# Kernel optimization log

Hardware: AMD Instinct MI355X
Metric: run time of the kernel (lower is better)

## Reference

```python
import jax, jax.numpy as jnp
import numpy as np

N_NODES = 100000
N_EDGES = 3200000
D_IN = 256   # module's size_out (input feature dim)
D_OUT = 128  # module's size_in (output feature dim)


def setup_inputs() -> dict:
    key = jax.random.key(0)
    k1, k2, k3, k4, k5 = jax.random.split(key, 5)
    x = jax.random.normal(k1, (N_NODES, D_IN), dtype=jnp.float32)
    W = jax.random.normal(k2, (D_IN, D_OUT), dtype=jnp.float32) * 0.05
    edge_src = jax.random.randint(k3, (N_EDGES,), 0, N_NODES, dtype=jnp.int32)
    edge_dst = jax.random.randint(k4, (N_EDGES,), 0, N_NODES, dtype=jnp.int32)
    edge_weight = jax.random.uniform(k5, (N_EDGES,), dtype=jnp.float32)
    return {"x": x, "W": W, "edge_src": edge_src, "edge_dst": edge_dst,
            "edge_weight": edge_weight}


def reference(x, W, edge_src, edge_dst, edge_weight):
    # dense projection: torch.mm(x, weights) -> [N, D_OUT]
    h = x @ W
    # sparse adjacency matmul: torch.spmm(A, h) with A in COO form
    # out[d] = sum_{e: dst_e = d} w_e * h[src_e]
    msgs = edge_weight[:, None] * h[edge_src]          # [E, D_OUT]
    out = jax.ops.segment_sum(msgs, edge_dst, num_segments=N_NODES)
    return out
```

## Files before the change

### kernel.cpp

```cpp
#include <hip/hip_runtime.h>

#define D_IN 256
#define D_OUT 128

typedef __bf16  bf16x8 __attribute__((ext_vector_type(8)));
typedef float   f32x4  __attribute__((ext_vector_type(4)));

__global__ __launch_bounds__(256) void wtrans_kernel(const float* __restrict__ W,
                                                     __bf16* __restrict__ Wt) {
    int n = blockIdx.x * 256 + threadIdx.x;
    int k = n >> 7;
    int col = n & 127;
    Wt[(size_t)col * D_IN + k] = (__bf16)W[(size_t)k * D_OUT + col];
}

__global__ __launch_bounds__(256) void gemm_mfma_kernel(const float* __restrict__ x,
                                                        const __bf16* __restrict__ Wt,
                                                        __bf16* __restrict__ h16, int M) {
    const int lane = threadIdx.x & 63;
    const int wid  = threadIdx.x >> 6;
    const int r0   = blockIdx.x * 128 + wid * 32;
    const int lr   = lane & 15;
    const int koff = (lane >> 4) * 8;

    int rowA = r0 + lr;        if (rowA >= M) rowA = M - 1;
    int rowB = r0 + 16 + lr;   if (rowB >= M) rowB = M - 1;
    const float* pa0 = &x[(size_t)rowA * D_IN + koff];
    const float* pa1 = &x[(size_t)rowB * D_IN + koff];

    f32x4 acc0[8], acc1[8];
#pragma unroll
    for (int c = 0; c < 8; ++c) { acc0[c] = (f32x4)0.f; acc1[c] = (f32x4)0.f; }

#pragma unroll
    for (int t = 0; t < 8; ++t) {
        float4 fa0 = *(const float4*)(pa0 + t * 32);
        float4 fa1 = *(const float4*)(pa0 + t * 32 + 4);
        float4 fb0 = *(const float4*)(pa1 + t * 32);
        float4 fb1 = *(const float4*)(pa1 + t * 32 + 4);
        bf16x8 aA, aB;
        aA[0]=(__bf16)fa0.x; aA[1]=(__bf16)fa0.y; aA[2]=(__bf16)fa0.z; aA[3]=(__bf16)fa0.w;
        aA[4]=(__bf16)fa1.x; aA[5]=(__bf16)fa1.y; aA[6]=(__bf16)fa1.z; aA[7]=(__bf16)fa1.w;
        aB[0]=(__bf16)fb0.x; aB[1]=(__bf16)fb0.y; aB[2]=(__bf16)fb0.z; aB[3]=(__bf16)fb0.w;
        aB[4]=(__bf16)fb1.x; aB[5]=(__bf16)fb1.y; aB[6]=(__bf16)fb1.z; aB[7]=(__bf16)fb1.w;
#pragma unroll
        for (int c = 0; c < 8; ++c) {
            bf16x8 b = *(const bf16x8*)&Wt[(size_t)(c * 16 + lr) * D_IN + t * 32 + koff];
            acc0[c] = __builtin_amdgcn_mfma_f32_16x16x32_bf16(aA, b, acc0[c], 0, 0, 0);
            acc1[c] = __builtin_amdgcn_mfma_f32_16x16x32_bf16(aB, b, acc1[c], 0, 0, 0);
        }
    }

    const int q = lane >> 4;
#pragma unroll
    for (int c = 0; c < 8; ++c) {
        int col = c * 16 + lr;
#pragma unroll
        for (int i = 0; i < 4; ++i) {
            int ra = r0 + q * 4 + i;
            int rb = r0 + 16 + q * 4 + i;
            if (ra < M) h16[(size_t)ra * D_OUT + col] = (__bf16)acc0[c][i];
            if (rb < M) h16[(size_t)rb * D_OUT + col] = (__bf16)acc1[c][i];
        }
    }
}

__global__ void hist_kernel(const int* __restrict__ dst, int* __restrict__ count, int E) {
    int i = blockIdx.x * blockDim.x + threadIdx.x;
    int stride = gridDim.x * blockDim.x;
    for (; i < E; i += stride) atomicAdd(&count[dst[i]], 1);
}

__global__ void scan1_kernel(const int* __restrict__ count, int* __restrict__ offsets,
                             int* __restrict__ bsum, int N) {
    __shared__ int s[256];
    int tid = threadIdx.x;
    int i = blockIdx.x * 256 + tid;
    int v = (i < N) ? count[i] : 0;
    s[tid] = v;
    __syncthreads();
    for (int off = 1; off < 256; off <<= 1) {
        int t = (tid >= off) ? s[tid - off] : 0;
        __syncthreads();
        s[tid] += t;
        __syncthreads();
    }
    if (i < N) offsets[i] = s[tid] - v;
    if (tid == 255) bsum[blockIdx.x] = s[255];
}

__global__ void scan2_kernel(const int* __restrict__ bsum, int* __restrict__ bscan, int NB) {
    __shared__ int s[512];
    int tid = threadIdx.x;
    int v = (tid < NB) ? bsum[tid] : 0;
    s[tid] = v;
    __syncthreads();
    for (int off = 1; off < 512; off <<= 1) {
        int t = (tid >= off) ? s[tid - off] : 0;
        __syncthreads();
        s[tid] += t;
        __syncthreads();
    }
    if (tid < NB) bscan[tid] = s[tid] - v;
}

__global__ void scan3_kernel(int* __restrict__ offsets, const int* __restrict__ bscan,
                             int* __restrict__ cursor, int N) {
    int i = blockIdx.x * blockDim.x + threadIdx.x;
    if (i < N) {
        int o = offsets[i] + bscan[i >> 8];
        offsets[i] = o;
        cursor[i]  = o;
    }
}

__global__ void scatter_kernel(const int* __restrict__ src, const int* __restrict__ dst,
                               const float* __restrict__ w, int* __restrict__ cursor,
                               int2* __restrict__ ep, int E) {
    int i = blockIdx.x * blockDim.x + threadIdx.x;
    int stride = gridDim.x * blockDim.x;
    for (; i < E; i += stride) {
        int d = dst[i];
        int pos = atomicAdd(&cursor[d], 1);
        ep[pos] = make_int2(src[i], __float_as_int(w[i]));
    }
}

__global__ __launch_bounds__(256) void spmm_kernel(const int* __restrict__ offsets,
                                                   const int* __restrict__ count,
                                                   const int2* __restrict__ ep,
                                                   const unsigned int* __restrict__ h16,
                                                   float* __restrict__ out, int N) {
    int wid  = (blockIdx.x * 256 + threadIdx.x) >> 6;
    int lane = threadIdx.x & 63;
    if (wid >= N) return;
    int start = offsets[wid];
    int cnt   = count[wid];
    float ax = 0.f, ay = 0.f;
    for (int j = 0; j < cnt; j += 8) {
        int2 e[8]; float wt[8];
#pragma unroll
        for (int k = 0; k < 8; ++k) {
            int jj = j + k;
            int idx = start + (jj < cnt ? jj : cnt - 1);
            e[k] = ep[idx];
            wt[k] = (jj < cnt) ? __int_as_float(e[k].y) : 0.f;
        }
        unsigned int u[8];
#pragma unroll
        for (int k = 0; k < 8; ++k)
            u[k] = h16[(size_t)e[k].x * 64 + lane];
#pragma unroll
        for (int k = 0; k < 8; ++k) {
            float flo = __uint_as_float(u[k] << 16);
            float fhi = __uint_as_float(u[k] & 0xffff0000u);
            ax += wt[k] * flo;
            ay += wt[k] * fhi;
        }
    }
    out[(size_t)wid * D_OUT + lane * 2 + 0] = ax;
    out[(size_t)wid * D_OUT + lane * 2 + 1] = ay;
}

__global__ __launch_bounds__(256) void edge_atomic_kernel(const int* __restrict__ src,
                                                          const int* __restrict__ dst,
                                                          const float* __restrict__ w,
                                                          const unsigned int* __restrict__ h16,
                                                          float* __restrict__ out, int E) {
    int wid  = (blockIdx.x * 256 + threadIdx.x) >> 6;
    int lane = threadIdx.x & 63;
    if (wid >= E) return;
    int s = src[wid], d = dst[wid];
    float ww = w[wid];
    unsigned int u = h16[(size_t)s * 64 + lane];
    atomicAdd(&out[(size_t)d * D_OUT + lane * 2 + 0], ww * __uint_as_float(u << 16));
    atomicAdd(&out[(size_t)d * D_OUT + lane * 2 + 1], ww * __uint_as_float(u & 0xffff0000u));
}

extern "C" void kernel_launch(void* const* d_in, const int* in_sizes, int n_in,
                              void* d_out, int out_size, void* d_ws, size_t ws_size,
                              hipStream_t stream) {
    const float* x    = (const float*)d_in[0];
    const float* W    = (const float*)d_in[1];
    const int*   esrc = (const int*)d_in[2];
    const int*   edst = (const int*)d_in[3];
    const float* ew   = (const float*)d_in[4];
    float* out = (float*)d_out;

    const int M = in_sizes[0] / D_IN;
    const int E = in_sizes[2];

    char* ws = (char*)d_ws;
    size_t off = 0;
    __bf16* h16    = (__bf16*)(ws + off); off += (size_t)M * D_OUT * 2;
    int2*   ep     = (int2*)  (ws + off); off += (size_t)E * 8;
    __bf16* Wt     = (__bf16*)(ws + off); off += (size_t)D_IN * D_OUT * 2;
    int*    offsets= (int*)   (ws + off); off += (size_t)M * 4;
    int*    count  = (int*)   (ws + off); off += (size_t)M * 4;
    int*    cursor = (int*)   (ws + off); off += (size_t)M * 4;
    int*    bsum   = (int*)   (ws + off); off += 2048;
    int*    bscan  = (int*)   (ws + off); off += 2048;
    const bool use_csr = (off <= ws_size);

    wtrans_kernel<<<(D_IN * D_OUT + 255) / 256, 256, 0, stream>>>(W, Wt);
    gemm_mfma_kernel<<<(M + 127) / 128, 256, 0, stream>>>(x, Wt, h16, M);

    if (use_csr) {
        int NB = (M + 255) / 256;
        hipMemsetAsync(count, 0, (size_t)M * 4, stream);
        hist_kernel  <<<2048, 256, 0, stream>>>(edst, count, E);
        scan1_kernel <<<NB, 256, 0, stream>>>(count, offsets, bsum, M);
        scan2_kernel <<<1, 512, 0, stream>>>(bsum, bscan, NB);
        scan3_kernel <<<NB, 256, 0, stream>>>(offsets, bscan, cursor, M);
        scatter_kernel<<<2048, 256, 0, stream>>>(esrc, edst, ew, cursor, ep, E);
        spmm_kernel  <<<(M + 3) / 4, 256, 0, stream>>>(offsets, count, ep,
                                                       (const unsigned int*)h16, out, M);
    } else {
        hipMemsetAsync(d_out, 0, (size_t)out_size * 4, stream);
        long long nthreads = (long long)E * 64;
        edge_atomic_kernel<<<(nthreads + 255) / 256, 256, 0, stream>>>(
            esrc, edst, ew, (const unsigned int*)h16, out, E);
    }
}
```

Before: 728.4 us.

## Record per-edge rank in histogram, make scatter atomic-free and XCD-partitioned by destination

The histogram pass now stores each edge's atomic return value as its rank within its destination segment, so the scatter pass computes positions as offsets[d]+rank[i] without a second round of atomics and the cursor array is dropped. Scatter blocks are split into 8 groups keyed on blockIdx&7, each owning a contiguous destination range, so that writes into ep from one group land in a localized region, presumably matching the XCD round-robin dispatch. Every group rereads the whole dst array, and an extra E-sized rank array is written and read. The SpMM inner loop is also unrolled from 8 to 16 edges per batch for more gathers in flight, at the cost of more wasted clamped loads on short rows and higher register pressure.

```diff
diff --git a/kernel.cpp b/kernel.cpp
--- a/kernel.cpp
+++ b/kernel.cpp
@@ -65,10 +65,11 @@
     }
 }
 
-__global__ void hist_kernel(const int* __restrict__ dst, int* __restrict__ count, int E) {
+__global__ void hist_kernel(const int* __restrict__ dst, int* __restrict__ count,
+                            int* __restrict__ rank, int E) {
     int i = blockIdx.x * blockDim.x + threadIdx.x;
     int stride = gridDim.x * blockDim.x;
-    for (; i < E; i += stride) atomicAdd(&count[dst[i]], 1);
+    for (; i < E; i += stride) rank[i] = atomicAdd(&count[dst[i]], 1);
 }
 
 __global__ void scan1_kernel(const int* __restrict__ count, int* __restrict__ offsets,
@@ -104,25 +105,29 @@
     if (tid < NB) bscan[tid] = s[tid] - v;
 }
 
-__global__ void scan3_kernel(int* __restrict__ offsets, const int* __restrict__ bscan,
-                             int* __restrict__ cursor, int N) {
+__global__ void scan3_kernel(int* __restrict__ offsets, const int* __restrict__ bscan, int N) {
     int i = blockIdx.x * blockDim.x + threadIdx.x;
-    if (i < N) {
-        int o = offsets[i] + bscan[i >> 8];
-        offsets[i] = o;
-        cursor[i]  = o;
-    }
-}
-
-__global__ void scatter_kernel(const int* __restrict__ src, const int* __restrict__ dst,
-                               const float* __restrict__ w, int* __restrict__ cursor,
-                               int2* __restrict__ ep, int E) {
-    int i = blockIdx.x * blockDim.x + threadIdx.x;
-    int stride = gridDim.x * blockDim.x;
-    for (; i < E; i += stride) {
+    if (i < N) offsets[i] += bscan[i >> 8];
+}
+
+__global__ __launch_bounds__(256) void scatter_kernel(const int* __restrict__ src,
+                                                      const int* __restrict__ dst,
+                                                      const float* __restrict__ w,
+                                                      const int* __restrict__ rank,
+                                                      const int* __restrict__ offsets,
+                                                      int2* __restrict__ ep,
+                                                      int E, int npx, int CS) {
+    const int xcd   = blockIdx.x & 7;
+    const int chunk = blockIdx.x >> 3;
+    const int lo = xcd * npx;
+    const int hi = lo + npx;
+    const int e1 = min(E, (chunk + 1) * CS);
+    for (int i = chunk * CS + threadIdx.x; i < e1; i += 256) {
         int d = dst[i];
-        int pos = atomicAdd(&cursor[d], 1);
-        ep[pos] = make_int2(src[i], __float_as_int(w[i]));
+        if (d >= lo && d < hi) {
+            int pos = offsets[d] + rank[i];
+            ep[pos] = make_int2(src[i], __float_as_int(w[i]));
+        }
     }
 }
 
@@ -137,25 +142,23 @@
     int start = offsets[wid];
     int cnt   = count[wid];
     float ax = 0.f, ay = 0.f;
-    for (int j = 0; j < cnt; j += 8) {
-        int2 e[8]; float wt[8];
-#pragma unroll
-        for (int k = 0; k < 8; ++k) {
+    for (int j = 0; j < cnt; j += 16) {
+        int2 e[16]; float wt[16];
+#pragma unroll
+        for (int k = 0; k < 16; ++k) {
             int jj = j + k;
             int idx = start + (jj < cnt ? jj : cnt - 1);
             e[k] = ep[idx];
             wt[k] = (jj < cnt) ? __int_as_float(e[k].y) : 0.f;
         }
-        unsigned int u[8];
-#pragma unroll
-        for (int k = 0; k < 8; ++k)
+        unsigned int u[16];
+#pragma unroll
+        for (int k = 0; k < 16; ++k)
             u[k] = h16[(size_t)e[k].x * 64 + lane];
 #pragma unroll
-        for (int k = 0; k < 8; ++k) {
-            float flo = __uint_as_float(u[k] << 16);
-            float fhi = __uint_as_float(u[k] & 0xffff0000u);
-            ax += wt[k] * flo;
-            ay += wt[k] * fhi;
+        for (int k = 0; k < 16; ++k) {
+            ax += wt[k] * __uint_as_float(u[k] << 16);
+            ay += wt[k] * __uint_as_float(u[k] & 0xffff0000u);
         }
     }
     out[(size_t)wid * D_OUT + lane * 2 + 0] = ax;
@@ -194,10 +197,10 @@
     size_t off = 0;
     __bf16* h16    = (__bf16*)(ws + off); off += (size_t)M * D_OUT * 2;
     int2*   ep     = (int2*)  (ws + off); off += (size_t)E * 8;
+    int*    rank   = (int*)   (ws + off); off += (size_t)E * 4;
     __bf16* Wt     = (__bf16*)(ws + off); off += (size_t)D_IN * D_OUT * 2;
     int*    offsets= (int*)   (ws + off); off += (size_t)M * 4;
     int*    count  = (int*)   (ws + off); off += (size_t)M * 4;
-    int*    cursor = (int*)   (ws + off); off += (size_t)M * 4;
     int*    bsum   = (int*)   (ws + off); off += 2048;
     int*    bscan  = (int*)   (ws + off); off += 2048;
     const bool use_csr = (off <= ws_size);
@@ -208,11 +211,16 @@
     if (use_csr) {
         int NB = (M + 255) / 256;
         hipMemsetAsync(count, 0, (size_t)M * 4, stream);
-        hist_kernel  <<<2048, 256, 0, stream>>>(edst, count, E);
+        hist_kernel  <<<2048, 256, 0, stream>>>(edst, count, rank, E);
         scan1_kernel <<<NB, 256, 0, stream>>>(count, offsets, bsum, M);
         scan2_kernel <<<1, 512, 0, stream>>>(bsum, bscan, NB);
-        scan3_kernel <<<NB, 256, 0, stream>>>(offsets, bscan, cursor, M);
-        scatter_kernel<<<2048, 256, 0, stream>>>(esrc, edst, ew, cursor, ep, E);
+        scan3_kernel <<<NB, 256, 0, stream>>>(offsets, bscan, M);
+
+        const int NCHUNK = 256;
+        const int CS  = (E + NCHUNK - 1) / NCHUNK;
+        const int npx = (M + 7) / 8;
+        scatter_kernel<<<NCHUNK * 8, 256, 0, stream>>>(esrc, edst, ew, rank, offsets,
+                                                       ep, E, npx, CS);
         spmm_kernel  <<<(M + 3) / 4, 256, 0, stream>>>(offsets, count, ep,
                                                        (const unsigned int*)h16, out, M);
     } else {
```

Result: faster. 602.7 us (-17.3%).
